# Performance work log

Hardware: AMD Instinct MI355X
Metric: run time of the kernel (lower is better)

## Reference

```python
import jax, jax.numpy as jnp
import numpy as np

DIM = 768
HEADS = 8
HEAD_DIM = DIM // HEADS
SCALE = HEAD_DIM ** -0.5
EPS = 1e-5


def layernorm(x, gamma, beta):
    mu = jnp.mean(x, axis=-1, keepdims=True)
    var = jnp.mean((x - mu) ** 2, axis=-1, keepdims=True)
    return (x - mu) * jax.lax.rsqrt(var + EPS) * gamma + beta


def setup_inputs() -> dict:
    key = jax.random.key(0)
    ks = jax.random.split(key, 12)
    B, L, M, D = 8, 1024, 1024, DIM
    s = D ** -0.5
    return {
        "x": jax.random.normal(ks[0], (B, L, D), jnp.float32),
        "context": jax.random.normal(ks[1], (B, M, D), jnp.float32),
        "Wq": jax.random.normal(ks[2], (D, D), jnp.float32) * s,
        "bq": jnp.zeros((D,), jnp.float32),
        "Wkv": jax.random.normal(ks[3], (D, 2 * D), jnp.float32) * s,
        "bkv": jnp.zeros((2 * D,), jnp.float32),
        "Wp": jax.random.normal(ks[4], (D, D), jnp.float32) * s,
        "bp": jnp.zeros((D,), jnp.float32),
        "g1": jnp.ones((D,), jnp.float32),
        "b1": jnp.zeros((D,), jnp.float32),
        "g2": jnp.ones((D,), jnp.float32),
        "b2": jnp.zeros((D,), jnp.float32),
    }


def reference(x, context, Wq, bq, Wkv, bkv, Wp, bp, g1, b1, g2, b2):
    B, L, D = x.shape
    M = context.shape[1]
    Hp = Wp_ = int(L ** 0.5)
    x_n = layernorm(x, g1, b1)
    c_n = layernorm(context, g2, b2)
    q = (x_n @ Wq + bq).reshape(B, L, HEADS, HEAD_DIM).transpose(0, 2, 1, 3)  # bhld
    kv = (c_n @ Wkv + bkv).reshape(B, M, 2, HEADS, HEAD_DIM).transpose(2, 0, 3, 1, 4)
    k, v = kv[0], kv[1]  # bhmd
    attn = jnp.einsum("bhld,bhmd->bhlm", q, k) * SCALE
    w = jax.nn.softmax(attn, axis=-1)
    attn_map = w.mean(axis=1).sum(axis=-1).reshape(B, Hp, Wp_)
    out = jnp.einsum("bhlm,bhmd->bhld", w, v).transpose(0, 2, 1, 3).reshape(B, L, D)
    out = out @ Wp + bp
    # dropout is identity in eval mode (training=False)
    return out + x, attn_map
```

## Files before the change

kernel.cpp:

```cpp
#include <hip/hip_runtime.h>

typedef unsigned short u16;
typedef short bf16x8 __attribute__((ext_vector_type(8)));
typedef float f32x4 __attribute__((ext_vector_type(4)));
typedef unsigned short u16x8 __attribute__((ext_vector_type(8)));
typedef unsigned short u16x4 __attribute__((ext_vector_type(4)));

union bfr { unsigned int u[4]; bf16x8 v; };

__device__ __forceinline__ u16 f2bf(float f) {
    unsigned int u = __builtin_bit_cast(unsigned int, f);
    u = (u + 0x7fffu + ((u >> 16) & 1u)) >> 16;
    return (u16)u;
}

__device__ __forceinline__ unsigned int cvtpk(float lo, float hi) {
    unsigned int r;
    asm("v_cvt_pk_bf16_f32 %0, %1, %2" : "=v"(r) : "v"(lo), "v"(hi));
    return r;
}

__device__ __forceinline__ void gload16(const u16* src, u16* lds_dst) {
    __builtin_amdgcn_global_load_lds(
        (const __attribute__((address_space(1))) unsigned int*)src,
        (__attribute__((address_space(3))) unsigned int*)lds_dst, 16, 0, 0);
}

__global__ __launch_bounds__(256) void prep_ln_k(
    const float* __restrict__ x, const float* __restrict__ ctx,
    const float* __restrict__ g1, const float* __restrict__ b1,
    const float* __restrict__ g2, const float* __restrict__ b2,
    const float* __restrict__ Wq, const float* __restrict__ Wkv,
    const float* __restrict__ Wp,
    u16* __restrict__ xn, u16* __restrict__ cn,
    u16* __restrict__ WqT, u16* __restrict__ WkvT, u16* __restrict__ WpT)
{
    const int id = blockIdx.x;
    const int t = threadIdx.x;
    if (id >= 16384) {
        __shared__ float T[64][65];
        int t2 = id - 16384;
        const float* src; u16* dst; int lds, k0, n0;
        if (t2 < 288) { src = Wkv; dst = WkvT; lds = 1536; k0 = (t2 / 24) * 64; n0 = (t2 % 24) * 64; }
        else if (t2 < 432) { int u = t2 - 288; src = Wq; dst = WqT; lds = 768; k0 = (u / 12) * 64; n0 = (u % 12) * 64; }
        else { int u = t2 - 432; src = Wp; dst = WpT; lds = 768; k0 = (u / 12) * 64; n0 = (u % 12) * 64; }
        const int rr = t >> 4, c4 = (t & 15) * 4;
        #pragma unroll
        for (int it = 0; it < 4; it++) {
            int r = rr + it * 16;
            f32x4 v = *(const f32x4*)&src[(long)(k0 + r) * lds + n0 + c4];
            #pragma unroll
            for (int j = 0; j < 4; j++) T[c4 + j][r] = v[j];
        }
        __syncthreads();
        #pragma unroll
        for (int it = 0; it < 4; it++) {
            int r = rr + it * 16;
            u16x4 w;
            #pragma unroll
            for (int j = 0; j < 4; j++) w[j] = f2bf(T[r][c4 + j]);
            *(u16x4*)&dst[(long)(n0 + r) * 768 + k0 + c4] = w;
        }
        return;
    }
    const float* src; const float* g; const float* b; u16* dst;
    if (id < 8192) { src = x + (long)id * 768; g = g1; b = b1; dst = xn + (long)id * 768; }
    else { int r = id - 8192; src = ctx + (long)r * 768; g = g2; b = b2; dst = cn + (long)r * 768; }

    int lane = t & 63, wid = t >> 6;
    float v0 = src[t], v1 = src[t + 256], v2 = src[t + 512];
    float s = v0 + v1 + v2;
    for (int o = 32; o; o >>= 1) s += __shfl_xor(s, o);
    __shared__ float r1[4], r2[4];
    if (!lane) r1[wid] = s;
    __syncthreads();
    float mu = (r1[0] + r1[1] + r1[2] + r1[3]) * (1.0f / 768.0f);
    float d0 = v0 - mu, d1 = v1 - mu, d2 = v2 - mu;
    float q = d0 * d0 + d1 * d1 + d2 * d2;
    for (int o = 32; o; o >>= 1) q += __shfl_xor(q, o);
    if (!lane) r2[wid] = q;
    __syncthreads();
    float var = (r2[0] + r2[1] + r2[2] + r2[3]) * (1.0f / 768.0f);
    float rs = rsqrtf(var + 1e-5f);
    dst[t]       = f2bf(d0 * rs * g[t]       + b[t]);
    dst[t + 256] = f2bf(d1 * rs * g[t + 256] + b[t + 256]);
    dst[t + 512] = f2bf(d2 * rs * g[t + 512] + b[t + 512]);
}

#define GSTAGE(BUF, T) do {                                          \
    const int k0_ = (T) * 32;                                        \
    _Pragma("unroll")                                                \
    for (int c_ = 0; c_ < 2; c_++) {                                 \
        gload16(srcA[c_] + k0_, &As[BUF][ldsOff[c_]]);               \
        gload16(srcB[c_] + k0_, &Bs[BUF][ldsOff[c_]]);               \
    }                                                                \
} while (0)

#define GCOMP(BUF) do {                                              \
    bf16x8 av_[4], bv_[4];                                           \
    _Pragma("unroll")                                                \
    for (int m_ = 0; m_ < 4; m_++)                                   \
        av_[m_] = *(const bf16x8*)&As[BUF][(wr * 64 + m_ * 16 + i15) * 32 + g * 8]; \
    _Pragma("unroll")                                                \
    for (int n_ = 0; n_ < 4; n_++)                                   \
        bv_[n_] = *(const bf16x8*)&Bs[BUF][(wc * 64 + n_ * 16 + i15) * 32 + g * 8]; \
    _Pragma("unroll")                                                \
    for (int m_ = 0; m_ < 4; m_++)                                   \
        _Pragma("unroll")                                            \
        for (int n_ = 0; n_ < 4; n_++)                               \
            acc[m_][n_] = __builtin_amdgcn_mfma_f32_16x16x32_bf16(av_[m_], bv_[n_], acc[m_][n_], 0, 0, 0); \
} while (0)

#define GSTEP(T) do {                                                \
    if ((T) < 23) asm volatile("s_waitcnt vmcnt(4)" ::: "memory");   \
    else          asm volatile("s_waitcnt vmcnt(0)" ::: "memory");   \
    __builtin_amdgcn_s_barrier();                                    \
    __builtin_amdgcn_sched_barrier(0);                               \
    if ((T) + 2 < 24) GSTAGE(((T) + 2) % 3, (T) + 2);                \
    GCOMP((T) % 3);                                                  \
} while (0)

__global__ __launch_bounds__(256) void qkv_k(
    const u16* __restrict__ xn, const u16* __restrict__ cn,
    const u16* __restrict__ WqT, const u16* __restrict__ WkvT,
    const float* __restrict__ bq, const float* __restrict__ bkv,
    u16* __restrict__ Qb, u16* __restrict__ Kb, u16* __restrict__ Vt)
{
    __shared__ u16 As[3][128 * 32];
    __shared__ u16 Bs[3][128 * 32];
    const int id = blockIdx.x;
    const int swz = (id & 7) * 144 + (id >> 3);
    const int tid = threadIdx.x, lane = tid & 63, wid = tid >> 6;
    const int wr = wid >> 1, wc = wid & 1;
    const int g = lane >> 4, i15 = lane & 15;

    const bool isQ = swz < 384;
    int rt, ct;
    const u16* A; const u16* Bt; const float* bias;
    if (isQ) { rt = swz / 6;  ct = swz % 6;  A = xn; Bt = WqT;  bias = bq; }
    else { int s2 = swz - 384; rt = s2 / 12; ct = s2 % 12; A = cn; Bt = WkvT; bias = bkv; }
    const int row0 = rt * 128, col0 = ct * 128;

    const u16* srcA[2]; const u16* srcB[2]; int ldsOff[2];
    #pragma unroll
    for (int c = 0; c < 2; c++) {
        int P0 = (wid * 2 + c) * 1024;
        int P = P0 + lane * 16;
        int r = P >> 6, colx = (P & 63) >> 1;
        srcA[c] = A  + (long)(row0 + r) * 768 + colx;
        srcB[c] = Bt + (long)(col0 + r) * 768 + colx;
        ldsOff[c] = P0 >> 1;
    }

    f32x4 acc[4][4] = {};

    GSTAGE(0, 0);
    GSTAGE(1, 1);
    #pragma unroll
    for (int t = 0; t < 24; t++) GSTEP(t);

    float bv4[4];
    #pragma unroll
    for (int n = 0; n < 4; n++) bv4[n] = bias[col0 + wc * 64 + n * 16 + i15];

    #pragma unroll
    for (int m = 0; m < 4; m++) {
        #pragma unroll
        for (int n = 0; n < 4; n++) {
            const int col = col0 + wc * 64 + n * 16 + i15;
            #pragma unroll
            for (int r = 0; r < 4; r++) {
                const int row = row0 + wr * 64 + m * 16 + g * 4 + r;
                float v = acc[m][n][r];
                if (isQ) {
                    v = (v + bv4[n]) * 0.14724444706f;
                    int b = row >> 10, l = row & 1023;
                    int h = col / 96, d = col % 96;
                    Qb[((long)(b * 8 + h) * 1024 + l) * 96 + d] = f2bf(v);
                } else {
                    v += bv4[n];
                    int b = row >> 10, mt = row & 1023;
                    if (col < 768) {
                        int h = col / 96, d = col % 96;
                        Kb[((long)(b * 8 + h) * 1024 + mt) * 96 + d] = f2bf(v);
                    } else {
                        int cc = col - 768;
                        int h = cc / 96, d = cc % 96;
                        Vt[((long)(b * 8 + h) * 96 + d) * 1024 + mt] = f2bf(v);
                    }
                }
            }
        }
    }
}

__global__ __launch_bounds__(256) void flash_k(
    const u16* __restrict__ Qb, const u16* __restrict__ Kb,
    const u16* __restrict__ Vt, u16* __restrict__ Ob)
{
    const int i = blockIdx.x;
    const int s8 = i >> 3;
    const int bh = (i & 7) * 8 + (s8 >> 4);
    const int qt = s8 & 15;
    const int tid = threadIdx.x, lane = tid & 63, wid = tid >> 6;
    const int g = lane >> 4, i15 = lane & 15;

    __shared__ u16 Ks[2][6144];
    __shared__ u16 Vs[2][6144];

    const long baseQK = (long)bh * 98304;
    const u16* Kt  = Kb + baseQK;
    const u16* Vtp = Vt + baseQK;

    bf16x8 qf[3];
    {
        const u16* qrow = Qb + baseQK + (long)(qt * 64 + wid * 16 + i15) * 96 + g * 8;
        qf[0] = *(const bf16x8*)(qrow);
        qf[1] = *(const bf16x8*)(qrow + 32);
        qf[2] = *(const bf16x8*)(qrow + 64);
    }

    int krd[4];
    #pragma unroll
    for (int n = 0; n < 4; n++) {
        int q4 = i15 >> 2, rr = i15 & 3, m = n >> 1;
        int R = (n & 1) ? (m * 32 + ((q4 ^ 2) << 3) + 4 + rr)
                        : (m * 32 + (q4 << 3) + rr);
        krd[n] = R * 32 + g * 8;
    }
    int vrd[6][2];
    #pragma unroll
    for (int n6 = 0; n6 < 6; n6++) {
        int row = n6 * 16 + i15;
        #pragma unroll
        for (int kk = 0; kk < 2; kk++)
            vrd[n6][kk] = row * 64 + ((kk * 32 + g * 8) ^ ((row & 7) << 3));
    }

    int kgo[3], kwr[3], vgo[3], vwr[3];
    #pragma unroll
    for (int it = 0; it < 3; it++) {
        int e = tid + it * 256;
        int r = e / 12, cEl = (e % 12) * 8;
        kgo[it] = r * 96 + cEl;
        kwr[it] = (cEl >> 5) * 2048 + r * 32 + (cEl & 31);
        int d = e >> 3, m8 = (e & 7) * 8;
        vgo[it] = d * 1024 + m8;
        vwr[it] = d * 64 + (m8 ^ ((d & 7) << 3));
    }

    u16x8 kreg[3], vreg[3];
    #pragma unroll
    for (int it = 0; it < 3; it++) {
        kreg[it] = *(const u16x8*)&Kt[kgo[it]];
        vreg[it] = *(const u16x8*)&Vtp[vgo[it]];
    }
    #pragma unroll
    for (int it = 0; it < 3; it++) {
        *(u16x8*)&Ks[0][kwr[it]] = kreg[it];
        *(u16x8*)&Vs[0][vwr[it]] = vreg[it];
    }

    f32x4 o[6] = {};
    float lsum = 0.f;
    int cur = 0;

    for (int t = 0; t < 16; t++) {
        __syncthreads();
        if (t < 15) {
            #pragma unroll
            for (int it = 0; it < 3; it++) {
                kreg[it] = *(const u16x8*)&Kt[(t + 1) * 6144 + kgo[it]];
                vreg[it] = *(const u16x8*)&Vtp[(t + 1) * 64 + vgo[it]];
            }
        }

        f32x4 s[4] = {};
        #pragma unroll
        for (int kd = 0; kd < 3; kd++) {
            #pragma unroll
            for (int n = 0; n < 4; n++) {
                bf16x8 kf = *(const bf16x8*)&Ks[cur][kd * 2048 + krd[n]];
                s[n] = __builtin_amdgcn_mfma_f32_16x16x32_bf16(kf, qf[kd], s[n], 0, 0, 0);
            }
        }

        unsigned int pk[4][2];
        #pragma unroll
        for (int n = 0; n < 4; n++) {
            float p0 = exp2f(s[n][0]), p1 = exp2f(s[n][1]);
            float p2 = exp2f(s[n][2]), p3 = exp2f(s[n][3]);
            lsum += (p0 + p1) + (p2 + p3);
            pk[n][0] = cvtpk(p0, p1);
            pk[n][1] = cvtpk(p2, p3);
        }

        #pragma unroll
        for (int kk = 0; kk < 2; kk++) {
            bfr pa;
            pa.u[0] = pk[kk * 2][0];
            pa.u[1] = pk[kk * 2][1];
            pa.u[2] = __shfl_xor(pk[kk * 2 + 1][0], 32);
            pa.u[3] = __shfl_xor(pk[kk * 2 + 1][1], 32);
            #pragma unroll
            for (int n6 = 0; n6 < 6; n6++) {
                bf16x8 vf = *(const bf16x8*)&Vs[cur][vrd[n6][kk]];
                o[n6] = __builtin_amdgcn_mfma_f32_16x16x32_bf16(pa.v, vf, o[n6], 0, 0, 0);
            }
        }

        if (t < 15) {
            #pragma unroll
            for (int it = 0; it < 3; it++) {
                *(u16x8*)&Ks[cur ^ 1][kwr[it]] = kreg[it];
                *(u16x8*)&Vs[cur ^ 1][vwr[it]] = vreg[it];
            }
        }
        cur ^= 1;
    }

    lsum += __shfl_xor(lsum, 16);
    lsum += __shfl_xor(lsum, 32);
    float linv = 1.0f / lsum;

    const int b = bh >> 3, h = bh & 7;
    #pragma unroll
    for (int r = 0; r < 4; r++) {
        float lr = __shfl(linv, g * 4 + r);
        int row = qt * 64 + wid * 16 + g * 4 + r;
        long base = ((long)(b * 1024 + row)) * 768 + h * 96;
        #pragma unroll
        for (int n6 = 0; n6 < 6; n6++)
            Ob[base + n6 * 16 + i15] = f2bf(o[n6][r] * lr);
    }
}

__global__ __launch_bounds__(256) void out_k(
    const u16* __restrict__ Ob, const u16* __restrict__ WpT,
    const float* __restrict__ bp, const float* __restrict__ resid,
    float* __restrict__ out, float* __restrict__ amap)
{
    const int id = blockIdx.x;
    if (id >= 384) {
        amap[(id - 384) * 256 + threadIdx.x] = 1.0f;
        return;
    }
    __shared__ u16 As[3][128 * 32];
    __shared__ u16 Bs[3][128 * 32];
    const int swz = (id & 7) * 48 + (id >> 3);
    const int rt = swz / 6, ct = swz % 6;
    const int row0 = rt * 128, col0 = ct * 128;
    const int tid = threadIdx.x, lane = tid & 63, wid = tid >> 6;
    const int wr = wid >> 1, wc = wid & 1;
    const int g = lane >> 4, i15 = lane & 15;

    const u16* srcA[2]; const u16* srcB[2]; int ldsOff[2];
    #pragma unroll
    for (int c = 0; c < 2; c++) {
        int P0 = (wid * 2 + c) * 1024;
        int P = P0 + lane * 16;
        int r = P >> 6, colx = (P & 63) >> 1;
        srcA[c] = Ob  + (long)(row0 + r) * 768 + colx;
        srcB[c] = WpT + (long)(col0 + r) * 768 + colx;
        ldsOff[c] = P0 >> 1;
    }

    f32x4 acc[4][4] = {};

    GSTAGE(0, 0);
    GSTAGE(1, 1);
    #pragma unroll
    for (int t = 0; t < 24; t++) GSTEP(t);

    float bv4[4];
    #pragma unroll
    for (int n = 0; n < 4; n++) bv4[n] = bp[col0 + wc * 64 + n * 16 + i15];

    #pragma unroll
    for (int m = 0; m < 4; m++) {
        #pragma unroll
        for (int n = 0; n < 4; n++) {
            const int col = col0 + wc * 64 + n * 16 + i15;
            #pragma unroll
            for (int r = 0; r < 4; r++) {
                const int row = row0 + wr * 64 + m * 16 + g * 4 + r;
                long idx = (long)row * 768 + col;
                out[idx] = acc[m][n][r] + bv4[n] + resid[idx];
            }
        }
    }
}

extern "C" void kernel_launch(void* const* d_in, const int* in_sizes, int n_in,
                              void* d_out, int out_size, void* d_ws, size_t ws_size,
                              hipStream_t stream)
{
    const float* x   = (const float*)d_in[0];
    const float* ctx = (const float*)d_in[1];
    const float* Wq  = (const float*)d_in[2];
    const float* bq  = (const float*)d_in[3];
    const float* Wkv = (const float*)d_in[4];
    const float* bkv = (const float*)d_in[5];
    const float* Wp  = (const float*)d_in[6];
    const float* bp  = (const float*)d_in[7];
    const float* g1  = (const float*)d_in[8];
    const float* b1  = (const float*)d_in[9];
    const float* g2  = (const float*)d_in[10];
    const float* b2  = (const float*)d_in[11];
    float* out = (float*)d_out;

    char* w = (char*)d_ws;
    const long SZ_ROWS = 8192L * 768 * 2;
    long off = 0;
    u16* xn   = (u16*)(w + off); off += SZ_ROWS;
    u16* cn   = (u16*)(w + off); off += SZ_ROWS;
    u16* WqT  = (u16*)(w + off); off += 768L * 768 * 2;
    u16* WkvT = (u16*)(w + off); off += 1536L * 768 * 2;
    u16* WpT  = (u16*)(w + off); off += 768L * 768 * 2;
    u16* Qb   = (u16*)(w + off); off += SZ_ROWS;
    u16* Kb   = (u16*)(w + off); off += SZ_ROWS;
    u16* Vt   = (u16*)(w + off); off += SZ_ROWS;
    u16* Ob   = (u16*)(w + off); off += SZ_ROWS;

    prep_ln_k<<<16960, 256, 0, stream>>>(x, ctx, g1, b1, g2, b2, Wq, Wkv, Wp,
                                         xn, cn, WqT, WkvT, WpT);
    qkv_k<<<1152, 256, 0, stream>>>(xn, cn, WqT, WkvT, bq, bkv, Qb, Kb, Vt);
    flash_k<<<1024, 256, 0, stream>>>(Qb, Kb, Vt, Ob);
    out_k<<<416, 256, 0, stream>>>(Ob, WpT, bp, x, out, out + 6291456L);
}
```

Baseline: 161.1 us.

## Enlarge GEMM tiles to 256x128 with K=64 stages and swizzled LDS

The QKV and output projection GEMMs move from 128x128 tiles with K=32 and triple buffering to 256x128 tiles with K=64 and double buffering. LDS addresses are XOR-swizzled to avoid bank conflicts, and grid sizes are halved to match. The goal is more reuse per load, fewer barriers, and fewer bank conflicts. In exchange each block holds 8x4 accumulators (higher register pressure), LDS rises to 96KB per block, the pipeline waits on vmcnt(0) every step, and the out projection now launches only 192 GEMM blocks, which may underfill the 256 CUs.

```diff
diff --git a/kernel.cpp b/kernel.cpp
--- a/kernel.cpp
+++ b/kernel.cpp
@@ -87,38 +87,67 @@
     dst[t + 512] = f2bf(d2 * rs * g[t + 512] + b[t + 512]);
 }
 
-#define GSTAGE(BUF, T) do {                                          \
-    const int k0_ = (T) * 32;                                        \
+#define GSTAGE64(BUF, T) do {                                        \
+    const int k0_ = (T) * 64;                                        \
     _Pragma("unroll")                                                \
-    for (int c_ = 0; c_ < 2; c_++) {                                 \
-        gload16(srcA[c_] + k0_, &As[BUF][ldsOff[c_]]);               \
-        gload16(srcB[c_] + k0_, &Bs[BUF][ldsOff[c_]]);               \
+    for (int c_ = 0; c_ < 8; c_++)                                   \
+        gload16(srcA[c_] + k0_, &As[BUF][dstA[c_]]);                 \
+    _Pragma("unroll")                                                \
+    for (int c_ = 0; c_ < 4; c_++)                                   \
+        gload16(srcB[c_] + k0_, &Bs[BUF][dstB[c_]]);                 \
+} while (0)
+
+#define GCOMP64(BUF) do {                                            \
+    _Pragma("unroll")                                                \
+    for (int s_ = 0; s_ < 2; s_++) {                                 \
+        bf16x8 av_[8], bv_[4];                                       \
+        _Pragma("unroll")                                            \
+        for (int m_ = 0; m_ < 8; m_++)                               \
+            av_[m_] = *(const bf16x8*)&As[BUF][au[m_] + ca[s_]];     \
+        _Pragma("unroll")                                            \
+        for (int n_ = 0; n_ < 4; n_++)                               \
+            bv_[n_] = *(const bf16x8*)&Bs[BUF][bu[n_] + ca[s_]];     \
+        _Pragma("unroll")                                            \
+        for (int m_ = 0; m_ < 8; m_++)                               \
+            _Pragma("unroll")                                        \
+            for (int n_ = 0; n_ < 4; n_++)                           \
+                acc[m_][n_] = __builtin_amdgcn_mfma_f32_16x16x32_bf16(av_[m_], bv_[n_], acc[m_][n_], 0, 0, 0); \
     }                                                                \
 } while (0)
 
-#define GCOMP(BUF) do {                                              \
-    bf16x8 av_[4], bv_[4];                                           \
-    _Pragma("unroll")                                                \
-    for (int m_ = 0; m_ < 4; m_++)                                   \
-        av_[m_] = *(const bf16x8*)&As[BUF][(wr * 64 + m_ * 16 + i15) * 32 + g * 8]; \
-    _Pragma("unroll")                                                \
-    for (int n_ = 0; n_ < 4; n_++)                                   \
-        bv_[n_] = *(const bf16x8*)&Bs[BUF][(wc * 64 + n_ * 16 + i15) * 32 + g * 8]; \
-    _Pragma("unroll")                                                \
-    for (int m_ = 0; m_ < 4; m_++)                                   \
-        _Pragma("unroll")                                            \
-        for (int n_ = 0; n_ < 4; n_++)                               \
-            acc[m_][n_] = __builtin_amdgcn_mfma_f32_16x16x32_bf16(av_[m_], bv_[n_], acc[m_][n_], 0, 0, 0); \
-} while (0)
-
-#define GSTEP(T) do {                                                \
-    if ((T) < 23) asm volatile("s_waitcnt vmcnt(4)" ::: "memory");   \
-    else          asm volatile("s_waitcnt vmcnt(0)" ::: "memory");   \
+#define GSTEP64(T) do {                                              \
+    asm volatile("s_waitcnt vmcnt(0)" ::: "memory");                 \
     __builtin_amdgcn_s_barrier();                                    \
     __builtin_amdgcn_sched_barrier(0);                               \
-    if ((T) + 2 < 24) GSTAGE(((T) + 2) % 3, (T) + 2);                \
-    GCOMP((T) % 3);                                                  \
+    if ((T) + 1 < 12) GSTAGE64(((T) + 1) & 1, (T) + 1);              \
+    GCOMP64((T) & 1);                                                \
 } while (0)
+
+#define GSETUP64()                                                    \
+    const u16* srcA[8]; const u16* srcB[4];                           \
+    int dstA[8], dstB[4], au[8], bu[4], ca[2];                        \
+    {                                                                 \
+        const int swc = (((lane & 7) * 16) ^ ((lane >> 3) << 4)) >> 1;\
+        _Pragma("unroll")                                             \
+        for (int c = 0; c < 8; c++) {                                 \
+            dstA[c] = (wid * 8 + c) * 512;                            \
+            int rA = (wid * 8 + c) * 8 + (lane >> 3);                 \
+            srcA[c] = A + (long)(row0 + rA) * 768 + swc;              \
+        }                                                             \
+        _Pragma("unroll")                                             \
+        for (int c = 0; c < 4; c++) {                                 \
+            dstB[c] = (wid * 4 + c) * 512;                            \
+            int rB = (wid * 4 + c) * 8 + (lane >> 3);                 \
+            srcB[c] = Bt + (long)(col0 + rB) * 768 + swc;             \
+        }                                                             \
+        _Pragma("unroll")                                             \
+        for (int m = 0; m < 8; m++) au[m] = (wr * 128 + m * 16 + i15) * 64; \
+        _Pragma("unroll")                                             \
+        for (int n = 0; n < 4; n++) bu[n] = (wc * 64 + n * 16 + i15) * 64;  \
+        _Pragma("unroll")                                             \
+        for (int s = 0; s < 2; s++)                                   \
+            ca[s] = ((s * 64 + g * 16) ^ ((i15 & 7) << 4)) >> 1;      \
+    }
 
 __global__ __launch_bounds__(256) void qkv_k(
     const u16* __restrict__ xn, const u16* __restrict__ cn,
@@ -126,51 +155,41 @@
     const float* __restrict__ bq, const float* __restrict__ bkv,
     u16* __restrict__ Qb, u16* __restrict__ Kb, u16* __restrict__ Vt)
 {
-    __shared__ u16 As[3][128 * 32];
-    __shared__ u16 Bs[3][128 * 32];
+    __shared__ u16 As[2][256 * 64];
+    __shared__ u16 Bs[2][128 * 64];
     const int id = blockIdx.x;
-    const int swz = (id & 7) * 144 + (id >> 3);
+    const int swz = (id & 7) * 72 + (id >> 3);
     const int tid = threadIdx.x, lane = tid & 63, wid = tid >> 6;
     const int wr = wid >> 1, wc = wid & 1;
     const int g = lane >> 4, i15 = lane & 15;
 
-    const bool isQ = swz < 384;
+    const bool isQ = swz < 192;
     int rt, ct;
     const u16* A; const u16* Bt; const float* bias;
     if (isQ) { rt = swz / 6;  ct = swz % 6;  A = xn; Bt = WqT;  bias = bq; }
-    else { int s2 = swz - 384; rt = s2 / 12; ct = s2 % 12; A = cn; Bt = WkvT; bias = bkv; }
-    const int row0 = rt * 128, col0 = ct * 128;
-
-    const u16* srcA[2]; const u16* srcB[2]; int ldsOff[2];
-    #pragma unroll
-    for (int c = 0; c < 2; c++) {
-        int P0 = (wid * 2 + c) * 1024;
-        int P = P0 + lane * 16;
-        int r = P >> 6, colx = (P & 63) >> 1;
-        srcA[c] = A  + (long)(row0 + r) * 768 + colx;
-        srcB[c] = Bt + (long)(col0 + r) * 768 + colx;
-        ldsOff[c] = P0 >> 1;
-    }
-
-    f32x4 acc[4][4] = {};
-
-    GSTAGE(0, 0);
-    GSTAGE(1, 1);
-    #pragma unroll
-    for (int t = 0; t < 24; t++) GSTEP(t);
+    else { int s2 = swz - 192; rt = s2 / 12; ct = s2 % 12; A = cn; Bt = WkvT; bias = bkv; }
+    const int row0 = rt * 256, col0 = ct * 128;
+
+    GSETUP64();
+
+    f32x4 acc[8][4] = {};
+
+    GSTAGE64(0, 0);
+    #pragma unroll
+    for (int t = 0; t < 12; t++) GSTEP64(t);
 
     float bv4[4];
     #pragma unroll
     for (int n = 0; n < 4; n++) bv4[n] = bias[col0 + wc * 64 + n * 16 + i15];
 
     #pragma unroll
-    for (int m = 0; m < 4; m++) {
+    for (int m = 0; m < 8; m++) {
         #pragma unroll
         for (int n = 0; n < 4; n++) {
             const int col = col0 + wc * 64 + n * 16 + i15;
             #pragma unroll
             for (int r = 0; r < 4; r++) {
-                const int row = row0 + wr * 64 + m * 16 + g * 4 + r;
+                const int row = row0 + wr * 128 + m * 16 + g * 4 + r;
                 float v = acc[m][n][r];
                 if (isQ) {
                     v = (v + bv4[n]) * 0.14724444706f;
@@ -341,49 +360,41 @@
     float* __restrict__ out, float* __restrict__ amap)
 {
     const int id = blockIdx.x;
-    if (id >= 384) {
-        amap[(id - 384) * 256 + threadIdx.x] = 1.0f;
+    if (id >= 192) {
+        amap[(id - 192) * 256 + threadIdx.x] = 1.0f;
         return;
     }
-    __shared__ u16 As[3][128 * 32];
-    __shared__ u16 Bs[3][128 * 32];
-    const int swz = (id & 7) * 48 + (id >> 3);
+    __shared__ u16 As[2][256 * 64];
+    __shared__ u16 Bs[2][128 * 64];
+    const int swz = (id & 7) * 24 + (id >> 3);
     const int rt = swz / 6, ct = swz % 6;
-    const int row0 = rt * 128, col0 = ct * 128;
+    const int row0 = rt * 256, col0 = ct * 128;
     const int tid = threadIdx.x, lane = tid & 63, wid = tid >> 6;
     const int wr = wid >> 1, wc = wid & 1;
     const int g = lane >> 4, i15 = lane & 15;
 
-    const u16* srcA[2]; const u16* srcB[2]; int ldsOff[2];
-    #pragma unroll
-    for (int c = 0; c < 2; c++) {
-        int P0 = (wid * 2 + c) * 1024;
-        int P = P0 + lane * 16;
-        int r = P >> 6, colx = (P & 63) >> 1;
-        srcA[c] = Ob  + (long)(row0 + r) * 768 + colx;
-        srcB[c] = WpT + (long)(col0 + r) * 768 + colx;
-        ldsOff[c] = P0 >> 1;
-    }
-
-    f32x4 acc[4][4] = {};
-
-    GSTAGE(0, 0);
-    GSTAGE(1, 1);
-    #pragma unroll
-    for (int t = 0; t < 24; t++) GSTEP(t);
+    const u16* A = Ob; const u16* Bt = WpT;
+
+    GSETUP64();
+
+    f32x4 acc[8][4] = {};
+
+    GSTAGE64(0, 0);
+    #pragma unroll
+    for (int t = 0; t < 12; t++) GSTEP64(t);
 
     float bv4[4];
     #pragma unroll
     for (int n = 0; n < 4; n++) bv4[n] = bp[col0 + wc * 64 + n * 16 + i15];
 
     #pragma unroll
-    for (int m = 0; m < 4; m++) {
+    for (int m = 0; m < 8; m++) {
         #pragma unroll
         for (int n = 0; n < 4; n++) {
             const int col = col0 + wc * 64 + n * 16 + i15;
             #pragma unroll
             for (int r = 0; r < 4; r++) {
-                const int row = row0 + wr * 64 + m * 16 + g * 4 + r;
+                const int row = row0 + wr * 128 + m * 16 + g * 4 + r;
                 long idx = (long)row * 768 + col;
                 out[idx] = acc[m][n][r] + bv4[n] + resid[idx];
             }
@@ -424,7 +435,7 @@
 
     prep_ln_k<<<16960, 256, 0, stream>>>(x, ctx, g1, b1, g2, b2, Wq, Wkv, Wp,
                                          xn, cn, WqT, WkvT, WpT);
-    qkv_k<<<1152, 256, 0, stream>>>(xn, cn, WqT, WkvT, bq, bkv, Qb, Kb, Vt);
+    qkv_k<<<576, 256, 0, stream>>>(xn, cn, WqT, WkvT, bq, bkv, Qb, Kb, Vt);
     flash_k<<<1024, 256, 0, stream>>>(Qb, Kb, Vt, Ob);
-    out_k<<<416, 256, 0, stream>>>(Ob, WpT, bp, x, out, out + 6291456L);
-}
+    out_k<<<224, 256, 0, stream>>>(Ob, WpT, bp, x, out, out + 6291456L);
+}
```

Result: slower. 189.2 us (+17.4%).
